# Kernel tuning notes

Measured on AMD Instinct MI355X. Metric: run time of the kernel, lower is better.

The kernel has to match this reference:

```python
import jax, jax.numpy as jnp
import numpy as np
import math

B, S, D, H = 1, 2048, 2048, 16
DH = D // H  # 128
HALF = DH // 2  # 64


def setup_inputs() -> dict:
    key = jax.random.key(0)
    ks = jax.random.split(key, 6)
    x = jax.random.normal(ks[0], (B, S, D), dtype=jnp.float32)
    # rotary frequencies: freqs_cis = exp(i * t * theta), theta_j = 10000^{-2j/DH}
    inv_freq = 1.0 / (10000.0 ** (np.arange(0, DH, 2, dtype=np.float32) / DH))  # [HALF]
    t = np.arange(S, dtype=np.float32)
    angles = np.outer(t, inv_freq)  # [S, HALF]
    freqs_cos = jnp.asarray(np.cos(angles), dtype=jnp.float32)
    freqs_sin = jnp.asarray(np.sin(angles), dtype=jnp.float32)
    # additive causal mask [1,1,S,S]
    mask = jnp.triu(jnp.full((S, S), -1e9, dtype=jnp.float32), k=1)[None, None]
    scale = 0.02
    wq = jax.random.normal(ks[1], (D, D), dtype=jnp.float32) * scale
    wk = jax.random.normal(ks[2], (D, D), dtype=jnp.float32) * scale
    wv = jax.random.normal(ks[3], (D, D), dtype=jnp.float32) * scale
    wo = jax.random.normal(ks[4], (D, D), dtype=jnp.float32) * scale
    return {"x": x, "freqs_cos": freqs_cos, "freqs_sin": freqs_sin, "mask": mask,
            "wq": wq, "wk": wk, "wv": wv, "wo": wo, "start_pos": 0}


def _apply_rope(t, cos, sin):
    # t: [B,S,H,DH]; cos/sin: [S,HALF] broadcast as [1,S,1,HALF]
    tr = t.reshape(*t.shape[:-1], HALF, 2)
    even, odd = tr[..., 0], tr[..., 1]
    c = cos[None, :, None, :]
    s = sin[None, :, None, :]
    out_even = even * c - odd * s
    out_odd = even * s + odd * c
    return jnp.stack([out_even, out_odd], axis=-1).reshape(t.shape)


def reference(x, freqs_cos, freqs_sin, mask, wq, wk, wv, wo, start_pos):
    bsz, seqlen, _ = x.shape
    q = (x @ wq.T).reshape(bsz, seqlen, H, DH)
    k = (x @ wk.T).reshape(bsz, seqlen, H, DH)
    v = (x @ wv.T).reshape(bsz, seqlen, H, DH)
    q = _apply_rope(q, freqs_cos, freqs_sin)
    k = _apply_rope(k, freqs_cos, freqs_sin)
    q = q.transpose(0, 2, 1, 3)  # [B,H,S,DH]
    k = k.transpose(0, 2, 1, 3)
    v = v.transpose(0, 2, 1, 3)
    scores = jnp.einsum('bhqd,bhkd->bhqk', q, k) / math.sqrt(DH) + mask
    probs = jax.nn.softmax(scores, axis=-1)
    out = jnp.einsum('bhqk,bhkd->bhqd', probs, v)  # [B,H,S,DH]
    # faithful to original: transpose(2,3) then view(bsz, seqlen, dim)
    out = out.transpose(0, 1, 3, 2).reshape(bsz, seqlen, D)
    return out @ wo.T
```

## Files before the change

kernel.cpp:

```cpp
#include <hip/hip_runtime.h>

typedef unsigned short u16;
typedef unsigned int   u32;
typedef short  short8   __attribute__((ext_vector_type(8)));
typedef float  floatx4  __attribute__((ext_vector_type(4)));
typedef u16    ushortx2 __attribute__((ext_vector_type(2)));
typedef u16    ushortx4 __attribute__((ext_vector_type(4)));

__device__ __forceinline__ float bf2f(u16 u) {
  union { u32 i; float f; } v; v.i = ((u32)u) << 16; return v.f;
}
__device__ __forceinline__ u16 f2bf(float x) {
  union { float f; u32 i; } v; v.f = x;
  u32 r = v.i + 0x7FFFu + ((v.i >> 16) & 1u);
  return (u16)(r >> 16);
}

#if __has_builtin(__builtin_amdgcn_exp2f)
#define EXP2F(x) __builtin_amdgcn_exp2f(x)
#else
#define EXP2F(x) __exp2f(x)
#endif

#define GLOAD_LDS16(gptr, lptr)                                                   \
  __builtin_amdgcn_global_load_lds(                                               \
      (const __attribute__((address_space(1))) void*)(gptr),                      \
      (__attribute__((address_space(3))) void*)(lptr), 16, 0, 0)

#define WAITV(n) asm volatile("s_waitcnt vmcnt(" #n ")" ::: "memory")
#define WAITL    asm volatile("s_waitcnt lgkmcnt(0)" ::: "memory")
#define BAR      __builtin_amdgcn_s_barrier()

__global__ __launch_bounds__(256) void cvt_all(
    const floatx4* __restrict__ x,  const floatx4* __restrict__ wq,
    const floatx4* __restrict__ wk, const floatx4* __restrict__ wv,
    const floatx4* __restrict__ wo,
    ushortx4* __restrict__ xb, ushortx4* __restrict__ wqkv,
    ushortx4* __restrict__ wob) {
  int i = blockIdx.x * 256 + threadIdx.x;
  const floatx4* in; ushortx4* out;
  switch (blockIdx.y) {
    case 0:  in = x;  out = xb; break;
    case 1:  in = wq; out = wqkv; break;
    case 2:  in = wk; out = wqkv + (size_t)1048576; break;
    case 3:  in = wv; out = wqkv + (size_t)2097152; break;
    default: in = wo; out = wob; break;
  }
  floatx4 v = in[i];
  ushortx4 o;
  o.x = f2bf(v.x); o.y = f2bf(v.y); o.z = f2bf(v.z); o.w = f2bf(v.w);
  out[i] = o;
}

__global__ __launch_bounds__(512, 2) void gemm256_bt(
    const u16* __restrict__ A, const u16* __restrict__ B, u16* __restrict__ C,
    int N, int K, int lda, int ldb, int ldc) {
  const int cpx = gridDim.x >> 3;
  const int wg = ((int)blockIdx.x & 7) * cpx + ((int)blockIdx.x >> 3);
  const int ntn = N / 192;
  const int m0 = (wg / ntn) << 8;
  const int n0 = (wg % ntn) * 192;

  __shared__ __align__(16) u16 As[2][256][64];
  __shared__ __align__(16) u16 Bs[2][192][64];

  const int t = threadIdx.x;
  const int lane = t & 63;
  const int wave = t >> 6;
  const int wr = wave >> 2;
  const int wc = wave & 3;
  const int quad = lane >> 4;
  const int mrow = lane & 15;
  const int sw = mrow & 7;

  const int srow = lane >> 3;
  const int gso  = ((lane & 7) ^ srow) << 3;

  const u16* gA = A + (size_t)(m0 + (wave << 3) + srow) * lda + gso;
  const u16* gB = B + (size_t)(n0 + (wave << 3) + srow) * ldb + gso;

  floatx4 acc[8][3] = {};
  short8 afr[4][2], bfr[3][2];

  const int NT = K >> 6;

#define ST_A(nb, h, kt)                                                        \
  do {                                                                         \
    GLOAD_LDS16(gA + (size_t)((h) * 128) * lda + ((kt) << 6),                  \
                &As[nb][(h) * 128 + (wave << 3)][0]);                          \
    GLOAD_LDS16(gA + (size_t)((h) * 128 + 64) * lda + ((kt) << 6),             \
                &As[nb][(h) * 128 + 64 + (wave << 3)][0]);                     \
  } while (0)
#define ST_B1(nb, c, kt)                                                       \
  do {                                                                         \
    GLOAD_LDS16(gB + (size_t)((c) * 64) * ldb + ((kt) << 6),                   \
                &Bs[nb][(c) * 64 + (wave << 3)][0]);                           \
  } while (0)

#define LDA4(bf, base_row)                                                     \
  do {                                                                         \
    _Pragma("unroll") for (int i_ = 0; i_ < 4; i_++)                           \
      _Pragma("unroll") for (int kk_ = 0; kk_ < 2; kk_++)                      \
        afr[i_][kk_] = *(const short8*)&As[bf][(base_row) + (i_ << 4) + mrow]  \
                            [(((kk_ << 2) | quad) ^ sw) << 3];                 \
  } while (0)
#define LDB1(bf, j)                                                            \
  do {                                                                         \
    _Pragma("unroll") for (int kk_ = 0; kk_ < 2; kk_++)                        \
      bfr[j][kk_] = *(const short8*)&Bs[bf][(j) * 64 + (wc << 4) + mrow]       \
          [(((kk_ << 2) | quad) ^ sw) << 3];                                   \
  } while (0)
#define MMQ8(ilo, j)                                                           \
  do {                                                                         \
    __builtin_amdgcn_s_setprio(1);                                             \
    _Pragma("unroll") for (int kk_ = 0; kk_ < 2; kk_++)                        \
      _Pragma("unroll") for (int i_ = 0; i_ < 4; i_++)                         \
        acc[(ilo) + i_][j] = __builtin_amdgcn_mfma_f32_16x16x32_bf16(          \
            afr[i_][kk_], bfr[j][kk_], acc[(ilo) + i_][j], 0, 0, 0);           \
    __builtin_amdgcn_s_setprio(0);                                             \
  } while (0)

  ST_A(0, 0, 0); ST_B1(0, 0, 0); ST_B1(0, 1, 0); ST_B1(0, 2, 0); ST_A(0, 1, 0);
  WAITV(3);
  BAR;

  for (int kt = 0; kt < NT - 1; kt++) {
    const int bf = kt & 1, nb = bf ^ 1;
    LDA4(bf, (wr << 6));
    LDB1(bf, 0);
    LDB1(bf, 1);
    ST_A(nb, 0, kt + 1);
    ST_B1(nb, 0, kt + 1);
    WAITV(3);
    BAR;
    MMQ8(0, 0);
    MMQ8(0, 1);
    LDB1(bf, 2);
    ST_B1(nb, 1, kt + 1);
    ST_B1(nb, 2, kt + 1);
    BAR;
    MMQ8(0, 2);
    LDA4(bf, 128 + (wr << 6));
    MMQ8(4, 0);
    ST_A(nb, 1, kt + 1);
    WAITV(3);
    BAR;
    MMQ8(4, 1);
    MMQ8(4, 2);
  }
  {
    const int bf = (NT - 1) & 1;
    LDA4(bf, (wr << 6));
    LDB1(bf, 0);
    LDB1(bf, 1);
    WAITV(0);
    BAR;
    MMQ8(0, 0);
    MMQ8(0, 1);
    LDB1(bf, 2);
    BAR;
    MMQ8(0, 2);
    LDA4(bf, 128 + (wr << 6));
    MMQ8(4, 0);
    BAR;
    MMQ8(4, 1);
    MMQ8(4, 2);
  }

#pragma unroll
  for (int i = 0; i < 8; i++) {
    int row0 = m0 + ((i >= 4) ? 128 : 0) + (wr << 6) + ((i & 3) << 4) + (quad << 2);
#pragma unroll
    for (int j = 0; j < 3; j++) {
      int col = n0 + j * 64 + (wc << 4) + mrow;
#pragma unroll
      for (int r = 0; r < 4; r++)
        C[(size_t)(row0 + r) * ldc + col] = f2bf(acc[i][j][r]);
    }
  }
#undef ST_A
#undef ST_B1
#undef LDA4
#undef LDB1
#undef MMQ8
}

__global__ __launch_bounds__(256, 2) void gemm_out(
    const u16* __restrict__ A, const u16* __restrict__ B,
    float* __restrict__ C) {
  const int wg = ((int)blockIdx.x & 7) * 32 + ((int)blockIdx.x >> 3);
  const int m0 = (wg >> 4) << 7;
  const int n0 = (wg & 15) << 7;

  __shared__ __align__(16) u16 As[2][128][64];
  __shared__ __align__(16) u16 Bs[2][128][64];

  const int t = threadIdx.x;
  const int lane = t & 63;
  const int wave = t >> 6;
  const int wr = wave >> 1;
  const int wc = wave & 1;
  const int quad = lane >> 4;
  const int mrow = lane & 15;
  const int sw = mrow & 7;

  const int srow = lane >> 3;
  const int gso  = ((lane & 7) ^ srow) << 3;

  const u16* gA = A + (size_t)(m0 + (wave << 3) + srow) * 2048 + gso;
  const u16* gB = B + (size_t)(n0 + (wave << 3) + srow) * 2048 + gso;

  floatx4 acc[4][4] = {};
  short8 afr[4][2], bfr[4][2];

  const int NT = 32;

#define OST_A(nb, p, kt)                                                       \
  GLOAD_LDS16(gA + (size_t)((p) * 32) * 2048 + ((kt) << 6),                    \
              &As[nb][(p) * 32 + (wave << 3)][0])
#define OST_B(nb, p, kt)                                                       \
  GLOAD_LDS16(gB + (size_t)((p) * 32) * 2048 + ((kt) << 6),                    \
              &Bs[nb][(p) * 32 + (wave << 3)][0])

#define OLDA(bf)                                                               \
  do {                                                                         \
    _Pragma("unroll") for (int i_ = 0; i_ < 4; i_++)                           \
      _Pragma("unroll") for (int kk_ = 0; kk_ < 2; kk_++)                      \
        afr[i_][kk_] = *(const short8*)&As[bf][(wr << 6) + (i_ << 4) + mrow]   \
                            [(((kk_ << 2) | quad) ^ sw) << 3];                 \
  } while (0)
#define OLDB2(bf, jlo)                                                         \
  do {                                                                         \
    _Pragma("unroll") for (int j_ = 0; j_ < 2; j_++)                           \
      _Pragma("unroll") for (int kk_ = 0; kk_ < 2; kk_++)                      \
        bfr[(jlo) + j_][kk_] =                                                 \
            *(const short8*)&Bs[bf][(wc << 6) + (((jlo) + j_) << 4) + mrow]    \
                [(((kk_ << 2) | quad) ^ sw) << 3];                             \
  } while (0)
#define OMM16(jlo)                                                             \
  do {                                                                         \
    __builtin_amdgcn_s_setprio(1);                                             \
    _Pragma("unroll") for (int kk_ = 0; kk_ < 2; kk_++)                        \
      _Pragma("unroll") for (int i_ = 0; i_ < 4; i_++)                         \
        _Pragma("unroll") for (int j_ = 0; j_ < 2; j_++)                       \
          acc[i_][(jlo) + j_] = __builtin_amdgcn_mfma_f32_16x16x32_bf16(       \
              afr[i_][kk_], bfr[(jlo) + j_][kk_], acc[i_][(jlo) + j_], 0, 0, 0);\
    __builtin_amdgcn_s_setprio(0);                                             \
  } while (0)

  OST_A(0, 0, 0); OST_A(0, 1, 0); OST_A(0, 2, 0); OST_A(0, 3, 0);
  OST_B(0, 0, 0); OST_B(0, 2, 0); OST_B(0, 1, 0); OST_B(0, 3, 0);
  WAITV(2);
  BAR;

  for (int kt = 0; kt < NT - 1; kt++) {
    const int bf = kt & 1, nb = bf ^ 1;
    OLDA(bf);
    OLDB2(bf, 0);
    OST_A(nb, 0, kt + 1); OST_A(nb, 1, kt + 1);
    OST_A(nb, 2, kt + 1); OST_A(nb, 3, kt + 1);
    OST_B(nb, 0, kt + 1); OST_B(nb, 2, kt + 1);
    WAITV(6);
    BAR;
    OMM16(0);
    OLDB2(bf, 2);
    OST_B(nb, 1, kt + 1); OST_B(nb, 3, kt + 1);
    WAITV(2);
    BAR;
    OMM16(2);
  }
  {
    const int bf = (NT - 1) & 1;
    OLDA(bf);
    OLDB2(bf, 0);
    WAITV(0);
    BAR;
    OMM16(0);
    OLDB2(bf, 2);
    OMM16(2);
  }

#pragma unroll
  for (int i = 0; i < 4; i++) {
    int row0 = m0 + (wr << 6) + (i << 4) + (quad << 2);
#pragma unroll
    for (int j = 0; j < 4; j++) {
      int col = n0 + (wc << 6) + (j << 4) + mrow;
#pragma unroll
      for (int r = 0; r < 4; r++)
        C[(size_t)(row0 + r) * 2048 + col] = acc[i][j][r];
    }
  }
#undef OST_A
#undef OST_B
#undef OLDA
#undef OLDB2
#undef OMM16
}

__global__ __launch_bounds__(256) void rope_trans(
    u16* __restrict__ qkv, const float* __restrict__ cs,
    const float* __restrict__ sn, u16* __restrict__ vt) {
  __shared__ u16 tile[64][68];
  const int bx = blockIdx.x;
  if (bx < 16384) {
    const int isK = bx >> 13;
    int idx = (bx & 8191) * 256 + threadIdx.x;
    int p = idx & 63;
    int h = (idx >> 6) & 15;
    int s = idx >> 10;
    float c  = cs[(s << 6) | p];
    float si = sn[(s << 6) | p];
    float scale = isK ? 1.0f : 0.12751743f;
    size_t off = (size_t)s * 6144 + (isK ? 2048 : 0) + (h << 7) + (p << 1);
    ushortx2 eo = *(ushortx2*)(qkv + off);
    float e = bf2f(eo.x), o = bf2f(eo.y);
    ushortx2 r;
    r.x = f2bf((e * c - o * si) * scale);
    r.y = f2bf((e * si + o * c) * scale);
    *(ushortx2*)(qkv + off) = r;
  } else {
    const int b = bx - 16384;
    const u16* src = qkv + 4096;
    const int d0 = (b & 31) << 6;
    const int s0 = (b >> 5) << 6;
    const int tx = (threadIdx.x & 15) << 2;
    const int ty = threadIdx.x >> 4;
#pragma unroll
    for (int rr = 0; rr < 64; rr += 16) {
      ushortx4 v = *(const ushortx4*)(src + (size_t)(s0 + ty + rr) * 6144 + d0 + tx);
      *(ushortx4*)&tile[ty + rr][tx] = v;
    }
    __syncthreads();
#pragma unroll
    for (int rr = 0; rr < 64; rr += 16) {
      int r = ty + rr;
      ushortx4 o;
      o.x = tile[tx + 0][r]; o.y = tile[tx + 1][r];
      o.z = tile[tx + 2][r]; o.w = tile[tx + 3][r];
      *(ushortx4*)(vt + (size_t)(d0 + r) * 2048 + s0 + tx) = o;
    }
  }
}

__global__ __launch_bounds__(256, 2) void flash_attn(
    const u16* __restrict__ QKVp, const u16* __restrict__ VTp,
    u16* __restrict__ ATp) {
  const int r0id = (int)blockIdx.x + ((int)blockIdx.y << 5);
  const int h    = r0id & 15;
  const int qsub = 31 - (r0id >> 4);
  const int q0 = qsub << 6;
  const int ktmax = qsub >> 1;

  __shared__ __align__(16) u16 Ks[128][128];
  __shared__ __align__(16) u16 Vs[128][128];
  __shared__ __align__(16) u16 Ps[64][128];

  const int t = threadIdx.x;
  const int lane = t & 63;
  const int wave = t >> 6;
  const int quad = lane >> 4;
  const int mrow = lane & 15;
  const int sw   = mrow & 7;
  const int wmS = (wave & 1) << 5;
  const int wnS = (wave >> 1) << 6;
  const int wmV = (wave >> 1) << 6;
  const int wnP = (wave & 1) << 5;

  const int r4  = lane >> 4;
  const int seg = lane & 15;
  const int c0 = ((seg ^ r4) << 3);
  const int c4 = ((seg ^ (r4 + 4)) << 3);

  const u16* qbase = QKVp + (size_t)q0 * 6144 + (h << 7);
  const u16* kbase = QKVp + 2048 + (h << 7);
  const u16* vbase = VTp + (size_t)(h << 7) * 2048;

#define STAGE_K(kt)                                                            \
  do {                                                                         \
    int rr0_ = wave << 5;                                                      \
    _Pragma("unroll") for (int ii_ = 0; ii_ < 8; ii_++) {                      \
      int rr_ = rr0_ + (ii_ << 2);                                             \
      GLOAD_LDS16(kbase + (size_t)(((kt) << 7) + rr_ + r4) * 6144 +            \
                      ((ii_ & 1) ? c4 : c0),                                   \
                  &Ks[rr_][0]);                                                \
    }                                                                          \
  } while (0)
#define STAGE_V(kt)                                                            \
  do {                                                                         \
    int rr0_ = wave << 5;                                                      \
    _Pragma("unroll") for (int ii_ = 0; ii_ < 8; ii_++) {                      \
      int rr_ = rr0_ + (ii_ << 2);                                             \
      GLOAD_LDS16(vbase + (size_t)(rr_ + r4) * 2048 + ((kt) << 7) +            \
                      ((ii_ & 1) ? c4 : c0),                                   \
                  &Vs[rr_][0]);                                                \
    }                                                                          \
  } while (0)

  short8 aq[2][4];
#pragma unroll
  for (int i = 0; i < 2; i++)
#pragma unroll
    for (int kk = 0; kk < 4; kk++)
      aq[i][kk] = *(const short8*)(qbase + (size_t)(wmS + (i << 4) + mrow) * 6144 +
                                   (kk << 5) + (quad << 3));

  const short8 ones = {0x3F80, 0x3F80, 0x3F80, 0x3F80,
                       0x3F80, 0x3F80, 0x3F80, 0x3F80};

  floatx4 Oa[4][2] = {};
  floatx4 Oa1[2] = {};

  const float C2 = 23.083120654223414f;

  STAGE_K(0);
  STAGE_V(0);
  WAITV(8);
  BAR;

  for (int kt = 0; kt <= ktmax; kt++) {
    floatx4 sa[2][4] = {};
#pragma unroll
    for (int kk = 0; kk < 4; kk++) {
      short8 bk[4];
#pragma unroll
      for (int j = 0; j < 4; j++)
        bk[j] = *(const short8*)&Ks[wnS + (j << 4) + mrow][(((kk << 2) | quad) ^ sw) << 3];
      __builtin_amdgcn_s_setprio(1);
#pragma unroll
      for (int i = 0; i < 2; i++)
#pragma unroll
        for (int j = 0; j < 4; j++)
          sa[i][j] = __builtin_amdgcn_mfma_f32_16x16x32_bf16(aq[i][kk], bk[j], sa[i][j], 0, 0, 0);
      __builtin_amdgcn_s_setprio(0);
    }
    if (kt == ktmax) {
#pragma unroll
      for (int i = 0; i < 2; i++)
#pragma unroll
        for (int j = 0; j < 4; j++)
#pragma unroll
          for (int r = 0; r < 4; r++) {
            int ql = q0 + wmS + (i << 4) + (quad << 2) + r;
            int sl = (kt << 7) + wnS + (j << 4) + mrow;
            if (sl > ql) sa[i][j][r] = -1e30f;
          }
    }
#pragma unroll
    for (int i = 0; i < 2; i++)
#pragma unroll
      for (int j = 0; j < 4; j++)
#pragma unroll
        for (int r = 0; r < 4; r++) {
          int row = wmS + (i << 4) + (quad << 2) + r;
          int col = wnS + (j << 4) + mrow;
          Ps[row][((((col >> 3) ^ (row & 7)) << 3) | (col & 7))] =
              f2bf(EXP2F(sa[i][j][r] - C2));
        }
    WAITV(0);
    WAITL;
    BAR;

    if (kt < ktmax) STAGE_K(kt + 1);

#pragma unroll
    for (int kk = 0; kk < 4; kk++) {
      short8 av[4], bp[2];
#pragma unroll
      for (int i = 0; i < 4; i++)
        av[i] = *(const short8*)&Vs[wmV + (i << 4) + mrow][(((kk << 2) | quad) ^ sw) << 3];
#pragma unroll
      for (int j = 0; j < 2; j++)
        bp[j] = *(const short8*)&Ps[wnP + (j << 4) + mrow][(((kk << 2) | quad) ^ sw) << 3];
      __builtin_amdgcn_s_setprio(1);
#pragma unroll
      for (int i = 0; i < 4; i++)
#pragma unroll
        for (int j = 0; j < 2; j++)
          Oa[i][j] = __builtin_amdgcn_mfma_f32_16x16x32_bf16(av[i], bp[j], Oa[i][j], 0, 0, 0);
#pragma unroll
      for (int j = 0; j < 2; j++)
        Oa1[j] = __builtin_amdgcn_mfma_f32_16x16x32_bf16(ones, bp[j], Oa1[j], 0, 0, 0);
      __builtin_amdgcn_s_setprio(0);
    }
    WAITL;
    BAR;

    if (kt < ktmax) STAGE_V(kt + 1);
    WAITV(8);
    BAR;
  }
#undef STAGE_K
#undef STAGE_V

  float linv[2];
#pragma unroll
  for (int j = 0; j < 2; j++) linv[j] = 1.f / Oa1[j][0];
#pragma unroll
  for (int i = 0; i < 4; i++) {
    int drow = (h << 7) + wmV + (i << 4) + (quad << 2);
#pragma unroll
    for (int j = 0; j < 2; j++) {
      int col = q0 + wnP + (j << 4) + mrow;
#pragma unroll
      for (int r = 0; r < 4; r++)
        ATp[(size_t)(drow + r) * 2048 + col] = f2bf(Oa[i][j][r] * linv[j]);
    }
  }
}

extern "C" void kernel_launch(void* const* d_in, const int* in_sizes, int n_in,
                              void* d_out, int out_size, void* d_ws, size_t ws_size,
                              hipStream_t stream) {
  const float* x  = (const float*)d_in[0];
  const float* fc = (const float*)d_in[1];
  const float* fs = (const float*)d_in[2];
  const float* wq = (const float*)d_in[4];
  const float* wk = (const float*)d_in[5];
  const float* wv = (const float*)d_in[6];
  const float* wo = (const float*)d_in[7];
  float* out = (float*)d_out;

  char* ws = (char*)d_ws;
  const size_t MB = 1024 * 1024;
  u16*   XB   = (u16*)(ws + 0 * MB);
  u16*   WQKV = (u16*)(ws + 8 * MB);
  u16*   WOb  = (u16*)(ws + 32 * MB);
  u16*   QKV  = (u16*)(ws + 40 * MB);
  u16*   VT   = (u16*)(ws + 64 * MB);
  u16*   AT   = (u16*)(ws + 72 * MB);

  dim3 blk(256);
  cvt_all<<<dim3(4096, 5), blk, 0, stream>>>(
      (const floatx4*)x, (const floatx4*)wq, (const floatx4*)wk,
      (const floatx4*)wv, (const floatx4*)wo,
      (ushortx4*)XB, (ushortx4*)WQKV, (ushortx4*)WOb);

  gemm256_bt<<<dim3(256), dim3(512), 0, stream>>>(XB, WQKV, QKV,
                                                  6144, 2048, 2048, 2048, 6144);

  rope_trans<<<dim3(17408), blk, 0, stream>>>(QKV, fc, fs, VT);

  flash_attn<<<dim3(32, 16), blk, 0, stream>>>(QKV, VT, AT);

  gemm_out<<<dim3(256), blk, 0, stream>>>(AT, WOb, out);
}
```

Measured before the change: 266.7 us.

## Double-buffer K/V in flash attention, 8 waves, pair causal q-tiles per block

```diff
diff --git a/kernel.cpp b/kernel.cpp
--- a/kernel.cpp
+++ b/kernel.cpp
@@ -343,17 +343,15 @@
   }
 }
 
-__global__ __launch_bounds__(256, 2) void flash_attn(
+__global__ __launch_bounds__(512, 1) void flash_attn(
     const u16* __restrict__ QKVp, const u16* __restrict__ VTp,
     u16* __restrict__ ATp) {
-  const int r0id = (int)blockIdx.x + ((int)blockIdx.y << 5);
-  const int h    = r0id & 15;
-  const int qsub = 31 - (r0id >> 4);
-  const int q0 = qsub << 6;
-  const int ktmax = qsub >> 1;
-
-  __shared__ __align__(16) u16 Ks[128][128];
-  __shared__ __align__(16) u16 Vs[128][128];
+  const int bid = (int)blockIdx.x;
+  const int h   = bid & 15;
+  const int g   = bid >> 4;
+
+  __shared__ __align__(16) u16 Ks[2][128][128];
+  __shared__ __align__(16) u16 Vs[2][128][128];
   __shared__ __align__(16) u16 Ps[64][128];
 
   const int t = threadIdx.x;
@@ -363,8 +361,8 @@
   const int mrow = lane & 15;
   const int sw   = mrow & 7;
   const int wmS = (wave & 1) << 5;
-  const int wnS = (wave >> 1) << 6;
-  const int wmV = (wave >> 1) << 6;
+  const int wnS = (wave >> 1) << 5;
+  const int wmV = (wave >> 1) << 5;
   const int wnP = (wave & 1) << 5;
 
   const int r4  = lane >> 4;
@@ -372,141 +370,156 @@
   const int c0 = ((seg ^ r4) << 3);
   const int c4 = ((seg ^ (r4 + 4)) << 3);
 
-  const u16* qbase = QKVp + (size_t)q0 * 6144 + (h << 7);
   const u16* kbase = QKVp + 2048 + (h << 7);
   const u16* vbase = VTp + (size_t)(h << 7) * 2048;
 
-#define STAGE_K(kt)                                                            \
-  do {                                                                         \
-    int rr0_ = wave << 5;                                                      \
-    _Pragma("unroll") for (int ii_ = 0; ii_ < 8; ii_++) {                      \
+#define STAGE_K(nb, kt)                                                        \
+  do {                                                                         \
+    int rr0_ = wave << 4;                                                      \
+    _Pragma("unroll") for (int ii_ = 0; ii_ < 4; ii_++) {                      \
       int rr_ = rr0_ + (ii_ << 2);                                             \
       GLOAD_LDS16(kbase + (size_t)(((kt) << 7) + rr_ + r4) * 6144 +            \
                       ((ii_ & 1) ? c4 : c0),                                   \
-                  &Ks[rr_][0]);                                                \
+                  &Ks[nb][rr_][0]);                                            \
     }                                                                          \
   } while (0)
-#define STAGE_V(kt)                                                            \
-  do {                                                                         \
-    int rr0_ = wave << 5;                                                      \
-    _Pragma("unroll") for (int ii_ = 0; ii_ < 8; ii_++) {                      \
+#define STAGE_V(nb, kt)                                                        \
+  do {                                                                         \
+    int rr0_ = wave << 4;                                                      \
+    _Pragma("unroll") for (int ii_ = 0; ii_ < 4; ii_++) {                      \
       int rr_ = rr0_ + (ii_ << 2);                                             \
       GLOAD_LDS16(vbase + (size_t)(rr_ + r4) * 2048 + ((kt) << 7) +            \
                       ((ii_ & 1) ? c4 : c0),                                   \
-                  &Vs[rr_][0]);                                                \
+                  &Vs[nb][rr_][0]);                                            \
     }                                                                          \
   } while (0)
-
-  short8 aq[2][4];
-#pragma unroll
-  for (int i = 0; i < 2; i++)
-#pragma unroll
-    for (int kk = 0; kk < 4; kk++)
-      aq[i][kk] = *(const short8*)(qbase + (size_t)(wmS + (i << 4) + mrow) * 6144 +
-                                   (kk << 5) + (quad << 3));
 
   const short8 ones = {0x3F80, 0x3F80, 0x3F80, 0x3F80,
                        0x3F80, 0x3F80, 0x3F80, 0x3F80};
-
-  floatx4 Oa[4][2] = {};
-  floatx4 Oa1[2] = {};
-
   const float C2 = 23.083120654223414f;
 
-  STAGE_K(0);
-  STAGE_V(0);
-  WAITV(8);
-  BAR;
-
-  for (int kt = 0; kt <= ktmax; kt++) {
-    floatx4 sa[2][4] = {};
-#pragma unroll
-    for (int kk = 0; kk < 4; kk++) {
-      short8 bk[4];
-#pragma unroll
-      for (int j = 0; j < 4; j++)
-        bk[j] = *(const short8*)&Ks[wnS + (j << 4) + mrow][(((kk << 2) | quad) ^ sw) << 3];
-      __builtin_amdgcn_s_setprio(1);
+  for (int pass = 0; pass < 2; pass++) {
+    const int qsub  = pass ? g : 31 - g;
+    const int q0    = qsub << 6;
+    const int ktmax = qsub >> 1;
+    const u16* qbase = QKVp + (size_t)q0 * 6144 + (h << 7);
+
+    short8 aq[2][4];
+#pragma unroll
+    for (int i = 0; i < 2; i++)
+#pragma unroll
+      for (int kk = 0; kk < 4; kk++)
+        aq[i][kk] = *(const short8*)(qbase +
+                        (size_t)(wmS + (i << 4) + mrow) * 6144 +
+                        (kk << 5) + (quad << 3));
+
+    floatx4 Oa[2][2] = {};
+    floatx4 Oa1[2] = {};
+
+    STAGE_K(0, 0);
+    STAGE_V(0, 0);
+    WAITV(4);
+    BAR;
+
+    for (int kt = 0; kt <= ktmax; kt++) {
+      const int b = kt & 1, nb = b ^ 1;
+
+      floatx4 sa[2][2] = {};
+#pragma unroll
+      for (int kk = 0; kk < 4; kk++) {
+        short8 bk[2];
+#pragma unroll
+        for (int j = 0; j < 2; j++)
+          bk[j] = *(const short8*)&Ks[b][wnS + (j << 4) + mrow]
+                      [(((kk << 2) | quad) ^ sw) << 3];
+        __builtin_amdgcn_s_setprio(1);
+#pragma unroll
+        for (int i = 0; i < 2; i++)
+#pragma unroll
+          for (int j = 0; j < 2; j++)
+            sa[i][j] = __builtin_amdgcn_mfma_f32_16x16x32_bf16(
+                aq[i][kk], bk[j], sa[i][j], 0, 0, 0);
+        __builtin_amdgcn_s_setprio(0);
+      }
+
+      if (kt < ktmax) {
+        STAGE_K(nb, kt + 1);
+        STAGE_V(nb, kt + 1);
+      }
+
+      if (kt == ktmax) {
+#pragma unroll
+        for (int i = 0; i < 2; i++)
+#pragma unroll
+          for (int j = 0; j < 2; j++)
+#pragma unroll
+            for (int r = 0; r < 4; r++) {
+              int ql = q0 + wmS + (i << 4) + (quad << 2) + r;
+              int sl = (kt << 7) + wnS + (j << 4) + mrow;
+              if (sl > ql) sa[i][j][r] = -1e30f;
+            }
+      }
 #pragma unroll
       for (int i = 0; i < 2; i++)
 #pragma unroll
-        for (int j = 0; j < 4; j++)
-          sa[i][j] = __builtin_amdgcn_mfma_f32_16x16x32_bf16(aq[i][kk], bk[j], sa[i][j], 0, 0, 0);
-      __builtin_amdgcn_s_setprio(0);
+        for (int j = 0; j < 2; j++)
+#pragma unroll
+          for (int r = 0; r < 4; r++) {
+            int row = wmS + (i << 4) + (quad << 2) + r;
+            int col = wnS + (j << 4) + mrow;
+            Ps[row][((((col >> 3) ^ (row & 7)) << 3) | (col & 7))] =
+                f2bf(EXP2F(sa[i][j][r] - C2));
+          }
+      WAITL;
+      if (kt < ktmax) WAITV(8);
+      else            WAITV(0);
+      BAR;
+
+#pragma unroll
+      for (int kk = 0; kk < 4; kk++) {
+        short8 av[2], bp[2];
+#pragma unroll
+        for (int i = 0; i < 2; i++)
+          av[i] = *(const short8*)&Vs[b][wmV + (i << 4) + mrow]
+                      [(((kk << 2) | quad) ^ sw) << 3];
+#pragma unroll
+        for (int j = 0; j < 2; j++)
+          bp[j] = *(const short8*)&Ps[wnP + (j << 4) + mrow]
+                      [(((kk << 2) | quad) ^ sw) << 3];
+        __builtin_amdgcn_s_setprio(1);
+#pragma unroll
+        for (int i = 0; i < 2; i++)
+#pragma unroll
+          for (int j = 0; j < 2; j++)
+            Oa[i][j] = __builtin_amdgcn_mfma_f32_16x16x32_bf16(
+                av[i], bp[j], Oa[i][j], 0, 0, 0);
+#pragma unroll
+        for (int j = 0; j < 2; j++)
+          Oa1[j] = __builtin_amdgcn_mfma_f32_16x16x32_bf16(
+              ones, bp[j], Oa1[j], 0, 0, 0);
+        __builtin_amdgcn_s_setprio(0);
+      }
+      if (kt < ktmax) WAITV(4);
+      BAR;
     }
-    if (kt == ktmax) {
-#pragma unroll
-      for (int i = 0; i < 2; i++)
-#pragma unroll
-        for (int j = 0; j < 4; j++)
-#pragma unroll
-          for (int r = 0; r < 4; r++) {
-            int ql = q0 + wmS + (i << 4) + (quad << 2) + r;
-            int sl = (kt << 7) + wnS + (j << 4) + mrow;
-            if (sl > ql) sa[i][j][r] = -1e30f;
-          }
+
+    float linv[2];
+#pragma unroll
+    for (int j = 0; j < 2; j++) linv[j] = 1.f / Oa1[j][0];
+#pragma unroll
+    for (int i = 0; i < 2; i++) {
+      int drow = (h << 7) + wmV + (i << 4) + (quad << 2);
+#pragma unroll
+      for (int j = 0; j < 2; j++) {
+        int col = q0 + wnP + (j << 4) + mrow;
+#pragma unroll
+        for (int r = 0; r < 4; r++)
+          ATp[(size_t)(drow + r) * 2048 + col] = f2bf(Oa[i][j][r] * linv[j]);
+      }
     }
-#pragma unroll
-    for (int i = 0; i < 2; i++)
-#pragma unroll
-      for (int j = 0; j < 4; j++)
-#pragma unroll
-        for (int r = 0; r < 4; r++) {
-          int row = wmS + (i << 4) + (quad << 2) + r;
-          int col = wnS + (j << 4) + mrow;
-          Ps[row][((((col >> 3) ^ (row & 7)) << 3) | (col & 7))] =
-              f2bf(EXP2F(sa[i][j][r] - C2));
-        }
-    WAITV(0);
-    WAITL;
-    BAR;
-
-    if (kt < ktmax) STAGE_K(kt + 1);
-
-#pragma unroll
-    for (int kk = 0; kk < 4; kk++) {
-      short8 av[4], bp[2];
-#pragma unroll
-      for (int i = 0; i < 4; i++)
-        av[i] = *(const short8*)&Vs[wmV + (i << 4) + mrow][(((kk << 2) | quad) ^ sw) << 3];
-#pragma unroll
-      for (int j = 0; j < 2; j++)
-        bp[j] = *(const short8*)&Ps[wnP + (j << 4) + mrow][(((kk << 2) | quad) ^ sw) << 3];
-      __builtin_amdgcn_s_setprio(1);
-#pragma unroll
-      for (int i = 0; i < 4; i++)
-#pragma unroll
-        for (int j = 0; j < 2; j++)
-          Oa[i][j] = __builtin_amdgcn_mfma_f32_16x16x32_bf16(av[i], bp[j], Oa[i][j], 0, 0, 0);
-#pragma unroll
-      for (int j = 0; j < 2; j++)
-        Oa1[j] = __builtin_amdgcn_mfma_f32_16x16x32_bf16(ones, bp[j], Oa1[j], 0, 0, 0);
-      __builtin_amdgcn_s_setprio(0);
-    }
-    WAITL;
-    BAR;
-
-    if (kt < ktmax) STAGE_V(kt + 1);
-    WAITV(8);
-    BAR;
   }
 #undef STAGE_K
 #undef STAGE_V
-
-  float linv[2];
-#pragma unroll
-  for (int j = 0; j < 2; j++) linv[j] = 1.f / Oa1[j][0];
-#pragma unroll
-  for (int i = 0; i < 4; i++) {
-    int drow = (h << 7) + wmV + (i << 4) + (quad << 2);
-#pragma unroll
-    for (int j = 0; j < 2; j++) {
-      int col = q0 + wnP + (j << 4) + mrow;
-#pragma unroll
-      for (int r = 0; r < 4; r++)
-        ATp[(size_t)(drow + r) * 2048 + col] = f2bf(Oa[i][j][r] * linv[j]);
-    }
-  }
 }
 
 extern "C" void kernel_launch(void* const* d_in, const int* in_sizes, int n_in,
@@ -541,7 +554,7 @@
 
   rope_trans<<<dim3(17408), blk, 0, stream>>>(QKV, fc, fs, VT);
 
-  flash_attn<<<dim3(32, 16), blk, 0, stream>>>(QKV, VT, AT);
+  flash_attn<<<dim3(256), dim3(512), 0, stream>>>(QKV, VT, AT);
 
   gemm_out<<<dim3(256), blk, 0, stream>>>(AT, WOb, out);
 }
```

After: 266.3 us. No clear change (-0.2%).
